# Kernel tuning notes

Hardware: AMD Instinct MI355X
Metric: run time of the kernel (lower is better)

Reference implementation:

```python
import jax, jax.numpy as jnp
import numpy as np

B, SQ, SK, H, A = 4, 512, 512, 256, 128

def setup_inputs() -> dict:
    key = jax.random.key(0)
    ks = jax.random.split(key, 8)
    s = 1.0 / np.sqrt(H)
    sa = 1.0 / np.sqrt(A)
    return {
        "Q": jax.random.normal(ks[0], (B, SQ, H), dtype=jnp.float32),
        "K": jax.random.normal(ks[1], (B, SK, H), dtype=jnp.float32),
        "V": jax.random.normal(ks[2], (B, SK, H), dtype=jnp.float32),
        "W_q": jax.random.uniform(ks[3], (H, A), jnp.float32, -s, s),
        "W_k": jax.random.uniform(ks[4], (H, A), jnp.float32, -s, s),
        "v": jax.random.uniform(ks[5], (A,), jnp.float32, -sa, sa),
        "W_o": jax.random.uniform(ks[6], (H, H), jnp.float32, -s, s),
        "b_o": jax.random.uniform(ks[7], (H,), jnp.float32, -s, s),
    }

def reference(Q, K, V, W_q, W_k, v, W_o, b_o):
    # Q: (B, Sq, H), K/V: (B, Sk, H)
    Qt = Q @ W_q                      # (B, Sq, A)
    Kt = K @ W_k                      # (B, Sk, A)
    additive = jnp.tanh(Qt[:, :, None, :] + Kt[:, None, :, :])  # (B, Sq, Sk, A)
    scores = jnp.einsum('bqka,a->bqk', additive, v)             # (B, Sq, Sk)
    weights = jax.nn.softmax(scores, axis=-1)                   # (B, Sq, Sk)
    out = jnp.einsum('bqk,bkh->bqh', weights, V)                 # (B, Sq, H)
    out = out @ W_o + b_o
    return (out, weights)
```

## Files before the change

kernel.cpp:

```cpp
#include <hip/hip_runtime.h>
#include <math.h>

#define BB 4
#define SQL 512
#define SKL 512
#define HH 256
#define AA 128

#define PRESCALE 2.8853900817779268f

__device__ inline void fma4(float4& a, float s, const float4& b) {
    a.x = fmaf(s, b.x, a.x); a.y = fmaf(s, b.y, a.y);
    a.z = fmaf(s, b.z, a.z); a.w = fmaf(s, b.w, a.w);
}

__device__ inline unsigned short f_to_bf16(float f) {
    unsigned u = __float_as_uint(f);
    return (unsigned short)((u + 0x7fffu + ((u >> 16) & 1u)) >> 16);
}
__device__ inline float4 bf16x4_to_f4(uint2 u) {
    float4 r;
    r.x = __uint_as_float(u.x << 16);
    r.y = __uint_as_float(u.x & 0xffff0000u);
    r.z = __uint_as_float(u.y << 16);
    r.w = __uint_as_float(u.y & 0xffff0000u);
    return r;
}

__global__ __launch_bounds__(256) void prep_kernel(
    const float* __restrict__ Q, const float* __restrict__ K,
    const float* __restrict__ V,
    const float* __restrict__ Wq, const float* __restrict__ Wk,
    const float* __restrict__ Wo,
    float* __restrict__ Qt, float* __restrict__ Kt,
    unsigned short* __restrict__ VW)
{
    __shared__ float rows[16 * 260];
    __shared__ float wbuf[2][32 * 64];
    int tid = threadIdx.x;
    int bid = blockIdx.x;

    const float* X; const float* W;
    int ldW, col0, r0, kind;
    if (bid < 256)      { X=Q; W=Wq; ldW=AA; kind=0; r0=(bid>>1)*16;       col0=(bid&1)*64; }
    else if (bid < 512) { X=K; W=Wk; ldW=AA; kind=1; r0=((bid-256)>>1)*16; col0=((bid-256)&1)*64; }
    else { int b2=bid-512; X=V; W=Wo; ldW=HH; kind=2; r0=(b2>>2)*16;       col0=(b2&3)*64; }

    {
        const float4* Xv = (const float4*)(X + (size_t)r0 * HH);
        #pragma unroll
        for (int it = 0; it < 4; ++it) {
            int l = tid + it * 256;
            int rr = l >> 6, cc = (l & 63) << 2;
            *(float4*)&rows[rr * 260 + cc] = Xv[l];
        }
    }

    float4 wpf0, wpf1;
    {
        int l0 = tid, l1 = tid + 256;
        wpf0 = *(const float4*)(W + (size_t)(l0 >> 4) * ldW + col0 + ((l0 & 15) << 2));
        wpf1 = *(const float4*)(W + (size_t)(l1 >> 4) * ldW + col0 + ((l1 & 15) << 2));
    }

    int r  = tid >> 4;
    int c4 = tid & 15;
    float4 acc = {0.f, 0.f, 0.f, 0.f};

    for (int c = 0; c < 8; ++c) {
        {
            float4* wb = (float4*)&wbuf[c & 1][0];
            wb[tid]       = wpf0;
            wb[tid + 256] = wpf1;
            if (c < 7) {
                const float* Wb = W + (size_t)((c + 1) * 32) * ldW + col0;
                int l0 = tid, l1 = tid + 256;
                wpf0 = *(const float4*)(Wb + (size_t)(l0 >> 4) * ldW + ((l0 & 15) << 2));
                wpf1 = *(const float4*)(Wb + (size_t)(l1 >> 4) * ldW + ((l1 & 15) << 2));
            }
        }
        __syncthreads();
        const float* rrow = &rows[r * 260 + c * 32];
        const float* wb2  = &wbuf[c & 1][c4 << 2];
        #pragma unroll
        for (int h = 0; h < 32; ++h) {
            float rv  = rrow[h];
            float4 w4 = *(const float4*)(wb2 + h * 64);
            fma4(acc, rv, w4);
        }
    }

    if (kind < 2) {
        float* Y = (kind == 0) ? Qt : Kt;
        acc.x *= PRESCALE; acc.y *= PRESCALE; acc.z *= PRESCALE; acc.w *= PRESCALE;
        *(float4*)(Y + (size_t)(r0 + r) * AA + col0 + (c4 << 2)) = acc;
    } else {
        ushort4 s = { f_to_bf16(acc.x), f_to_bf16(acc.y),
                      f_to_bf16(acc.z), f_to_bf16(acc.w) };
        *(ushort4*)(VW + (size_t)(r0 + r) * HH + col0 + (c4 << 2)) = s;
    }
}

__global__ __launch_bounds__(256) void score_part(
    const float* __restrict__ Qt, const float* __restrict__ Kt,
    const float* __restrict__ v,  float* __restrict__ scores)
{
    __shared__ float sc[2][256];

    int tid = threadIdx.x;
    int bid = blockIdx.x;
    int b    = bid >> 9;
    int rem  = bid & 511;
    int q0   = rem & ~1;
    int half = rem & 1;
    int ag = tid & 15;
    int kl = tid >> 4;

    float q0r[8], dr[8], v2[8];
    {
        const float4* vp  = (const float4*)(v + ag * 8);
        const float4* qp0 = (const float4*)(Qt + (size_t)(b * SQL + q0)     * AA + ag * 8);
        const float4* qp1 = (const float4*)(Qt + (size_t)(b * SQL + q0 + 1) * AA + ag * 8);
        #pragma unroll
        for (int j4 = 0; j4 < 2; ++j4) {
            float4 vv4 = vp[j4];
            float4 a0  = qp0[j4];
            float4 a1  = qp1[j4];
            *(float4*)&q0r[j4 * 4] = a0;
            dr[j4*4+0] = __builtin_amdgcn_exp2f(a1.x - a0.x);
            dr[j4*4+1] = __builtin_amdgcn_exp2f(a1.y - a0.y);
            dr[j4*4+2] = __builtin_amdgcn_exp2f(a1.z - a0.z);
            dr[j4*4+3] = __builtin_amdgcn_exp2f(a1.w - a0.w);
            v2[j4*4+0] = 2.0f * vv4.x;
            v2[j4*4+1] = 2.0f * vv4.y;
            v2[j4*4+2] = 2.0f * vv4.z;
            v2[j4*4+3] = 2.0f * vv4.w;
        }
    }

    float S_all;
    {
        float ls = 0.f;
        #pragma unroll
        for (int j = 0; j < 8; ++j) ls += v2[j];
        ls += __shfl_xor(ls, 1);
        ls += __shfl_xor(ls, 2);
        ls += __shfl_xor(ls, 4);
        ls += __shfl_xor(ls, 8);
        S_all = 0.5f * ls;
    }

    const float4* kp = (const float4*)(Kt + (size_t)(b * SKL + half * 256 + kl) * AA + ag * 8);
    float4 n0 = kp[0], n1 = kp[1];
    for (int c = 0; c < 16; ++c) {
        float kt[8];
        *(float4*)&kt[0] = n0;
        *(float4*)&kt[4] = n1;
        if (c < 15) {
            const float4* np = kp + (size_t)(c + 1) * 16 * (AA / 4);
            n0 = np[0]; n1 = np[1];
        }
        float p0 = 0.f, p1 = 0.f;
        #pragma unroll
        for (int j = 0; j < 8; ++j) {
            float x0 = q0r[j] + kt[j];
            float e0 = __builtin_amdgcn_exp2f(x0);
            float e1 = e0 * dr[j];
            float r0 = __builtin_amdgcn_rcpf(e0 + 1.0f);
            float r1 = __builtin_amdgcn_rcpf(e1 + 1.0f);
            p0 = fmaf(v2[j], r0, p0);
            p1 = fmaf(v2[j], r1, p1);
        }
        p0 += __shfl_xor(p0, 1); p1 += __shfl_xor(p1, 1);
        p0 += __shfl_xor(p0, 2); p1 += __shfl_xor(p1, 2);
        p0 += __shfl_xor(p0, 4); p1 += __shfl_xor(p1, 4);
        p0 += __shfl_xor(p0, 8); p1 += __shfl_xor(p1, 8);
        if (ag == 0) {
            sc[0][c * 16 + kl] = S_all - p0;
            sc[1][c * 16 + kl] = S_all - p1;
        }
    }
    __syncthreads();

    if (tid < 128) {
        int q = tid >> 6, i = tid & 63;
        float4 val = *(float4*)&sc[q][i << 2];
        *(float4*)(scores + (size_t)(b * SQL + q0 + q) * SKL + half * 256 + (i << 2)) = val;
    }
}

__global__ __launch_bounds__(256) void softepi_kernel(
    const unsigned short* __restrict__ VW, const float* __restrict__ bo,
    float* __restrict__ weights, float* __restrict__ out)
{
    __shared__ float sw[2][SKL];
    __shared__ float pout[4][2][HH];
    __shared__ float pm[2][2], ps[2][2];

    int tid = threadIdx.x;
    int b  = blockIdx.x >> 8;
    int q0 = (blockIdx.x & 255) << 1;
    int wave = tid >> 6, lane = tid & 63;
    int qi = wave & 1, half = wave >> 1;

    {
        float* wrow = weights + (size_t)(b * SQL + q0 + qi) * SKL + half * 256;
        float4 sv = *(float4*)(wrow + (lane << 2));
        float m = fmaxf(fmaxf(sv.x, sv.y), fmaxf(sv.z, sv.w));
        #pragma unroll
        for (int off = 32; off; off >>= 1) m = fmaxf(m, __shfl_xor(m, off));
        if (lane == 0) pm[qi][half] = m;
        __syncthreads();
        float M = fmaxf(pm[qi][0], pm[qi][1]);
        float4 e;
        e.x = __builtin_amdgcn_exp2f((sv.x - M) * 1.44269504f);
        e.y = __builtin_amdgcn_exp2f((sv.y - M) * 1.44269504f);
        e.z = __builtin_amdgcn_exp2f((sv.z - M) * 1.44269504f);
        e.w = __builtin_amdgcn_exp2f((sv.w - M) * 1.44269504f);
        float s = (e.x + e.y) + (e.z + e.w);
        #pragma unroll
        for (int off = 32; off; off >>= 1) s += __shfl_xor(s, off);
        if (lane == 0) ps[qi][half] = s;
        __syncthreads();
        float rinv = 1.0f / (ps[qi][0] + ps[qi][1]);
        float4 w4 = { e.x * rinv, e.y * rinv, e.z * rinv, e.w * rinv };
        *(float4*)&sw[qi][half * 256 + (lane << 2)] = w4;
        *(float4*)(wrow + (lane << 2)) = w4;
    }
    __syncthreads();

    {
        const uint2* VWb = (const uint2*)(VW + (size_t)b * SKL * HH);
        float4 a0 = {0,0,0,0}, a1 = {0,0,0,0};
        int kbase = wave * 128;
        #pragma unroll 4
        for (int k = 0; k < 128; ++k) {
            int kk = kbase + k;
            uint2 u = VWb[(size_t)kk * (HH / 4) + lane];
            float4 vw4 = bf16x4_to_f4(u);
            float w0 = sw[0][kk];
            float w1 = sw[1][kk];
            fma4(a0, w0, vw4);
            fma4(a1, w1, vw4);
        }
        *(float4*)&pout[wave][0][lane << 2] = a0;
        *(float4*)&pout[wave][1][lane << 2] = a1;
    }
    __syncthreads();
    {
        int h = tid;
        float bias = bo[h];
        #pragma unroll
        for (int q2 = 0; q2 < 2; ++q2) {
            float s = bias + pout[0][q2][h] + pout[1][q2][h]
                           + pout[2][q2][h] + pout[3][q2][h];
            out[(size_t)(b * SQL + q0 + q2) * HH + h] = s;
        }
    }
}

extern "C" void kernel_launch(void* const* d_in, const int* in_sizes, int n_in,
                              void* d_out, int out_size, void* d_ws, size_t ws_size,
                              hipStream_t stream)
{
    const float* Q  = (const float*)d_in[0];
    const float* K  = (const float*)d_in[1];
    const float* V  = (const float*)d_in[2];
    const float* Wq = (const float*)d_in[3];
    const float* Wk = (const float*)d_in[4];
    const float* v  = (const float*)d_in[5];
    const float* Wo = (const float*)d_in[6];
    const float* bo = (const float*)d_in[7];

    float* out     = (float*)d_out;
    float* weights = out + (size_t)BB * SQL * HH;

    float* Qt = (float*)d_ws;
    float* Kt = Qt + (size_t)BB * SQL * AA;
    unsigned short* VW = (unsigned short*)(Kt + (size_t)BB * SKL * AA);

    prep_kernel <<<1024, 256, 0, stream>>>(Q, K, V, Wq, Wk, Wo, Qt, Kt, VW);
    score_part  <<<2048, 256, 0, stream>>>(Qt, Kt, v, weights);
    softepi_kernel<<<1024, 256, 0, stream>>>(VW, bo, weights, out);
}
```

Baseline: 130.8 us.

## Register-tile the projection GEMM and process four query rows per softmax block

The projection kernel now gives each thread a 4x4 output tile, with the input rows transposed in shared memory and weights double-buffered straight from global into registers. This replaces the old one-row-per-thread scheme that staged weights through shared memory and synchronised every chunk. The softmax/epilogue kernel now handles four query rows per block, one wave per row. This drops the cross-wave max/sum barriers and reuses each loaded V row across four queries. The cost is fewer blocks (256 and 512), which may leave the GPU under-occupied, plus more registers per thread.

```diff
diff --git a/kernel.cpp b/kernel.cpp
--- a/kernel.cpp
+++ b/kernel.cpp
@@ -35,69 +35,96 @@
     float* __restrict__ Qt, float* __restrict__ Kt,
     unsigned short* __restrict__ VW)
 {
-    __shared__ float rows[16 * 260];
-    __shared__ float wbuf[2][32 * 64];
+    __shared__ float rowsT[256 * 36];
     int tid = threadIdx.x;
     int bid = blockIdx.x;
 
     const float* X; const float* W;
     int ldW, col0, r0, kind;
-    if (bid < 256)      { X=Q; W=Wq; ldW=AA; kind=0; r0=(bid>>1)*16;       col0=(bid&1)*64; }
-    else if (bid < 512) { X=K; W=Wk; ldW=AA; kind=1; r0=((bid-256)>>1)*16; col0=((bid-256)&1)*64; }
-    else { int b2=bid-512; X=V; W=Wo; ldW=HH; kind=2; r0=(b2>>2)*16;       col0=(b2&3)*64; }
+    if (bid < 64)       { X=Q; W=Wq; ldW=AA; kind=0; r0=bid*32;      col0=0; }
+    else if (bid < 128) { X=K; W=Wk; ldW=AA; kind=1; r0=(bid-64)*32; col0=0; }
+    else { int b2=bid-128; X=V; W=Wo; ldW=HH; kind=2; r0=(b2>>1)*32; col0=(b2&1)*128; }
 
     {
         const float4* Xv = (const float4*)(X + (size_t)r0 * HH);
         #pragma unroll
-        for (int it = 0; it < 4; ++it) {
+        for (int it = 0; it < 8; ++it) {
             int l = tid + it * 256;
-            int rr = l >> 6, cc = (l & 63) << 2;
-            *(float4*)&rows[rr * 260 + cc] = Xv[l];
-        }
-    }
-
-    float4 wpf0, wpf1;
-    {
-        int l0 = tid, l1 = tid + 256;
-        wpf0 = *(const float4*)(W + (size_t)(l0 >> 4) * ldW + col0 + ((l0 & 15) << 2));
-        wpf1 = *(const float4*)(W + (size_t)(l1 >> 4) * ldW + col0 + ((l1 & 15) << 2));
-    }
-
-    int r  = tid >> 4;
-    int c4 = tid & 15;
-    float4 acc = {0.f, 0.f, 0.f, 0.f};
-
-    for (int c = 0; c < 8; ++c) {
+            int r = l >> 6, k4 = (l & 63) << 2;
+            float4 x = Xv[l];
+            rowsT[(k4 + 0) * 36 + r] = x.x;
+            rowsT[(k4 + 1) * 36 + r] = x.y;
+            rowsT[(k4 + 2) * 36 + r] = x.z;
+            rowsT[(k4 + 3) * 36 + r] = x.w;
+        }
+    }
+
+    int mg = tid >> 5;
+    int n4 = tid & 31;
+    int mbase = mg << 2;
+    const float* Wg = W + col0 + (n4 << 2);
+
+    float4 acc0 = {0,0,0,0}, acc1 = {0,0,0,0}, acc2 = {0,0,0,0}, acc3 = {0,0,0,0};
+    float4 wA[4], wB[4];
+    #pragma unroll
+    for (int j = 0; j < 4; ++j)
+        wA[j] = *(const float4*)(Wg + (size_t)j * ldW);
+    __syncthreads();
+
+    for (int g = 0; g < 64; g += 2) {
+        #pragma unroll
+        for (int j = 0; j < 4; ++j)
+            wB[j] = *(const float4*)(Wg + (size_t)((g + 1) * 4 + j) * ldW);
         {
-            float4* wb = (float4*)&wbuf[c & 1][0];
-            wb[tid]       = wpf0;
-            wb[tid + 256] = wpf1;
-            if (c < 7) {
-                const float* Wb = W + (size_t)((c + 1) * 32) * ldW + col0;
-                int l0 = tid, l1 = tid + 256;
-                wpf0 = *(const float4*)(Wb + (size_t)(l0 >> 4) * ldW + ((l0 & 15) << 2));
-                wpf1 = *(const float4*)(Wb + (size_t)(l1 >> 4) * ldW + ((l1 & 15) << 2));
+            float4 a[4];
+            #pragma unroll
+            for (int j = 0; j < 4; ++j)
+                a[j] = *(const float4*)&rowsT[(g * 4 + j) * 36 + mbase];
+            #pragma unroll
+            for (int j = 0; j < 4; ++j) {
+                fma4(acc0, a[j].x, wA[j]);
+                fma4(acc1, a[j].y, wA[j]);
+                fma4(acc2, a[j].z, wA[j]);
+                fma4(acc3, a[j].w, wA[j]);
             }
         }
-        __syncthreads();
-        const float* rrow = &rows[r * 260 + c * 32];
-        const float* wb2  = &wbuf[c & 1][c4 << 2];
-        #pragma unroll
-        for (int h = 0; h < 32; ++h) {
-            float rv  = rrow[h];
-            float4 w4 = *(const float4*)(wb2 + h * 64);
-            fma4(acc, rv, w4);
+        if (g + 2 < 64) {
+            #pragma unroll
+            for (int j = 0; j < 4; ++j)
+                wA[j] = *(const float4*)(Wg + (size_t)((g + 2) * 4 + j) * ldW);
+        }
+        {
+            float4 a[4];
+            #pragma unroll
+            for (int j = 0; j < 4; ++j)
+                a[j] = *(const float4*)&rowsT[((g + 1) * 4 + j) * 36 + mbase];
+            #pragma unroll
+            for (int j = 0; j < 4; ++j) {
+                fma4(acc0, a[j].x, wB[j]);
+                fma4(acc1, a[j].y, wB[j]);
+                fma4(acc2, a[j].z, wB[j]);
+                fma4(acc3, a[j].w, wB[j]);
+            }
         }
     }
 
     if (kind < 2) {
         float* Y = (kind == 0) ? Qt : Kt;
-        acc.x *= PRESCALE; acc.y *= PRESCALE; acc.z *= PRESCALE; acc.w *= PRESCALE;
-        *(float4*)(Y + (size_t)(r0 + r) * AA + col0 + (c4 << 2)) = acc;
+        float4 av[4] = {acc0, acc1, acc2, acc3};
+        #pragma unroll
+        for (int i = 0; i < 4; ++i) {
+            float4 s = av[i];
+            s.x *= PRESCALE; s.y *= PRESCALE; s.z *= PRESCALE; s.w *= PRESCALE;
+            *(float4*)(Y + (size_t)(r0 + mbase + i) * AA + (n4 << 2)) = s;
+        }
     } else {
-        ushort4 s = { f_to_bf16(acc.x), f_to_bf16(acc.y),
-                      f_to_bf16(acc.z), f_to_bf16(acc.w) };
-        *(ushort4*)(VW + (size_t)(r0 + r) * HH + col0 + (c4 << 2)) = s;
+        float4 av[4] = {acc0, acc1, acc2, acc3};
+        #pragma unroll
+        for (int i = 0; i < 4; ++i) {
+            ushort4 s = { f_to_bf16(av[i].x), f_to_bf16(av[i].y),
+                          f_to_bf16(av[i].z), f_to_bf16(av[i].w) };
+            *(ushort4*)(VW + (size_t)(r0 + mbase + i) * HH + col0 + (n4 << 2)) = s;
+        }
     }
 }
 
@@ -193,65 +220,75 @@
     const unsigned short* __restrict__ VW, const float* __restrict__ bo,
     float* __restrict__ weights, float* __restrict__ out)
 {
-    __shared__ float sw[2][SKL];
-    __shared__ float pout[4][2][HH];
-    __shared__ float pm[2][2], ps[2][2];
+    __shared__ float sw[4][SKL];
+    __shared__ float pout[4][4][HH];
 
     int tid = threadIdx.x;
-    int b  = blockIdx.x >> 8;
-    int q0 = (blockIdx.x & 255) << 1;
+    int b  = blockIdx.x >> 7;
+    int q0 = (blockIdx.x & 127) << 2;
     int wave = tid >> 6, lane = tid & 63;
-    int qi = wave & 1, half = wave >> 1;
-
-    {
-        float* wrow = weights + (size_t)(b * SQL + q0 + qi) * SKL + half * 256;
-        float4 sv = *(float4*)(wrow + (lane << 2));
-        float m = fmaxf(fmaxf(sv.x, sv.y), fmaxf(sv.z, sv.w));
+
+    {
+        float* wrow = weights + (size_t)(b * SQL + q0 + wave) * SKL;
+        float4 s0 = *(float4*)(wrow + (lane << 2));
+        float4 s1 = *(float4*)(wrow + 256 + (lane << 2));
+        float m = fmaxf(fmaxf(fmaxf(s0.x, s0.y), fmaxf(s0.z, s0.w)),
+                        fmaxf(fmaxf(s1.x, s1.y), fmaxf(s1.z, s1.w)));
         #pragma unroll
         for (int off = 32; off; off >>= 1) m = fmaxf(m, __shfl_xor(m, off));
-        if (lane == 0) pm[qi][half] = m;
-        __syncthreads();
-        float M = fmaxf(pm[qi][0], pm[qi][1]);
-        float4 e;
-        e.x = __builtin_amdgcn_exp2f((sv.x - M) * 1.44269504f);
-        e.y = __builtin_amdgcn_exp2f((sv.y - M) * 1.44269504f);
-        e.z = __builtin_amdgcn_exp2f((sv.z - M) * 1.44269504f);
-        e.w = __builtin_amdgcn_exp2f((sv.w - M) * 1.44269504f);
-        float s = (e.x + e.y) + (e.z + e.w);
+        float4 e0, e1;
+        e0.x = __builtin_amdgcn_exp2f((s0.x - m) * 1.44269504f);
+        e0.y = __builtin_amdgcn_exp2f((s0.y - m) * 1.44269504f);
+        e0.z = __builtin_amdgcn_exp2f((s0.z - m) * 1.44269504f);
+        e0.w = __builtin_amdgcn_exp2f((s0.w - m) * 1.44269504f);
+        e1.x = __builtin_amdgcn_exp2f((s1.x - m) * 1.44269504f);
+        e1.y = __builtin_amdgcn_exp2f((s1.y - m) * 1.44269504f);
+        e1.z = __builtin_amdgcn_exp2f((s1.z - m) * 1.44269504f);
+        e1.w = __builtin_amdgcn_exp2f((s1.w - m) * 1.44269504f);
+        float s = ((e0.x + e0.y) + (e0.z + e0.w)) + ((e1.x + e1.y) + (e1.z + e1.w));
         #pragma unroll
         for (int off = 32; off; off >>= 1) s += __shfl_xor(s, off);
-        if (lane == 0) ps[qi][half] = s;
-        __syncthreads();
-        float rinv = 1.0f / (ps[qi][0] + ps[qi][1]);
-        float4 w4 = { e.x * rinv, e.y * rinv, e.z * rinv, e.w * rinv };
-        *(float4*)&sw[qi][half * 256 + (lane << 2)] = w4;
-        *(float4*)(wrow + (lane << 2)) = w4;
+        float rinv = 1.0f / s;
+        float4 w0 = { e0.x * rinv, e0.y * rinv, e0.z * rinv, e0.w * rinv };
+        float4 w1 = { e1.x * rinv, e1.y * rinv, e1.z * rinv, e1.w * rinv };
+        *(float4*)&sw[wave][lane << 2]         = w0;
+        *(float4*)&sw[wave][256 + (lane << 2)] = w1;
+        *(float4*)(wrow + (lane << 2))       = w0;
+        *(float4*)(wrow + 256 + (lane << 2)) = w1;
     }
     __syncthreads();
 
     {
         const uint2* VWb = (const uint2*)(VW + (size_t)b * SKL * HH);
-        float4 a0 = {0,0,0,0}, a1 = {0,0,0,0};
+        float4 a0 = {0,0,0,0}, a1 = {0,0,0,0}, a2 = {0,0,0,0}, a3 = {0,0,0,0};
         int kbase = wave * 128;
-        #pragma unroll 4
-        for (int k = 0; k < 128; ++k) {
-            int kk = kbase + k;
-            uint2 u = VWb[(size_t)kk * (HH / 4) + lane];
-            float4 vw4 = bf16x4_to_f4(u);
-            float w0 = sw[0][kk];
-            float w1 = sw[1][kk];
-            fma4(a0, w0, vw4);
-            fma4(a1, w1, vw4);
+        for (int k4 = 0; k4 < 32; ++k4) {
+            int kk = kbase + k4 * 4;
+            float4 w0 = *(const float4*)&sw[0][kk];
+            float4 w1 = *(const float4*)&sw[1][kk];
+            float4 w2 = *(const float4*)&sw[2][kk];
+            float4 w3 = *(const float4*)&sw[3][kk];
+            #pragma unroll
+            for (int j = 0; j < 4; ++j) {
+                uint2 u = VWb[(size_t)(kk + j) * (HH / 4) + lane];
+                float4 vw4 = bf16x4_to_f4(u);
+                fma4(a0, ((const float*)&w0)[j], vw4);
+                fma4(a1, ((const float*)&w1)[j], vw4);
+                fma4(a2, ((const float*)&w2)[j], vw4);
+                fma4(a3, ((const float*)&w3)[j], vw4);
+            }
         }
         *(float4*)&pout[wave][0][lane << 2] = a0;
         *(float4*)&pout[wave][1][lane << 2] = a1;
+        *(float4*)&pout[wave][2][lane << 2] = a2;
+        *(float4*)&pout[wave][3][lane << 2] = a3;
     }
     __syncthreads();
     {
         int h = tid;
         float bias = bo[h];
         #pragma unroll
-        for (int q2 = 0; q2 < 2; ++q2) {
+        for (int q2 = 0; q2 < 4; ++q2) {
             float s = bias + pout[0][q2][h] + pout[1][q2][h]
                            + pout[2][q2][h] + pout[3][q2][h];
             out[(size_t)(b * SQL + q0 + q2) * HH + h] = s;
@@ -279,7 +316,7 @@
     float* Kt = Qt + (size_t)BB * SQL * AA;
     unsigned short* VW = (unsigned short*)(Kt + (size_t)BB * SKL * AA);
 
-    prep_kernel <<<1024, 256, 0, stream>>>(Q, K, V, Wq, Wk, Wo, Qt, Kt, VW);
-    score_part  <<<2048, 256, 0, stream>>>(Qt, Kt, v, weights);
-    softepi_kernel<<<1024, 256, 0, stream>>>(VW, bo, weights, out);
-}
+    prep_kernel  <<<256, 256, 0, stream>>>(Q, K, V, Wq, Wk, Wo, Qt, Kt, VW);
+    score_part   <<<2048, 256, 0, stream>>>(Qt, Kt, v, weights);
+    softepi_kernel<<<512, 256, 0, stream>>>(VW, bo, weights, out);
+}
```

New measurement: 130.0 us. About the same (-0.6%).
